# Kernel optimization log

Hardware: AMD Instinct MI355X
Metric: run time of the kernel (lower is better)

Reference implementation:

```python
import jax, jax.numpy as jnp
import numpy as np

PROB_THRESHOLD = 0.5


def setup_inputs() -> dict:
    key = jax.random.key(0)
    B, H, W = 64, 480, 864
    mask = jax.random.uniform(key, (B, H, W), dtype=jnp.float32)
    return {"mask": mask, "n_pts_threshold": 10, "n_bbox_loose_pixels": 64}


def reference(mask, n_pts_threshold, n_bbox_loose_pixels):
    """Threshold mask, find per-sample bbox of above-threshold pixels, loosen
    by n_bbox_loose_pixels, and emit a binary attention map over that bbox.
    If fewer than n_pts_threshold pixels fire, the whole frame is attended.
    Returns (att_map [B,H,W] float, bbox [B,4] int32 as [y0,y1,x0,x1])."""
    B, H, W = mask.shape
    binm = mask > PROB_THRESHOLD                       # [B,H,W] bool
    cnt = jnp.sum(binm, axis=(1, 2))                   # [B]

    rows = jnp.any(binm, axis=2)                       # [B,H] row has a hit
    cols = jnp.any(binm, axis=1)                       # [B,W] col has a hit
    r_idx = jnp.arange(H, dtype=jnp.int32)
    c_idx = jnp.arange(W, dtype=jnp.int32)

    min_r = jnp.min(jnp.where(rows, r_idx, H), axis=1)
    max_r = jnp.max(jnp.where(rows, r_idx, -1), axis=1)
    min_c = jnp.min(jnp.where(cols, c_idx, W), axis=1)
    max_c = jnp.max(jnp.where(cols, c_idx, -1), axis=1)

    loose = jnp.int32(n_bbox_loose_pixels)
    full = cnt < n_pts_threshold                       # too few pts -> full frame
    y0 = jnp.where(full, 0,     jnp.clip(min_r - loose, 0, H - 1))
    y1 = jnp.where(full, H - 1, jnp.clip(max_r + loose, 0, H - 1))
    x0 = jnp.where(full, 0,     jnp.clip(min_c - loose, 0, W - 1))
    x1 = jnp.where(full, W - 1, jnp.clip(max_c + loose, 0, W - 1))

    in_rows = (r_idx[None, :] >= y0[:, None]) & (r_idx[None, :] <= y1[:, None])  # [B,H]
    in_cols = (c_idx[None, :] >= x0[:, None]) & (c_idx[None, :] <= x1[:, None])  # [B,W]
    att_map = (in_rows[:, :, None] & in_cols[:, None, :]).astype(mask.dtype)     # [B,H,W]

    bbox = jnp.stack([y0, y1, x0, x1], axis=1).astype(jnp.int32)                 # [B,4]
    return att_map, bbox
```

## Files before the change

kernel.cpp:

```cpp
#include <hip/hip_runtime.h>

constexpr int B = 64;
constexpr int H = 480;
constexpr int W = 864;
constexpr float PROB_THRESHOLD = 0.5f;

constexpr int BPS = 16;
constexpr int ROWS_PER_BLK = H / BPS;
constexpr int W4 = W / 4;
constexpr int N4_PER_BLK = ROWS_PER_BLK * W4;
constexpr int NBLK = B * BPS;

using f32x4 = __attribute__((ext_vector_type(4))) float;
using u64 = unsigned long long;

constexpr u64 MARKER = 0xFFull << 56;

__device__ inline u64 pack_partial(int minr, int maxr, int minc, int maxc,
                                   int cnt) {
  u64 v = (u64)(unsigned)minr | ((u64)(unsigned)(maxr + 1) << 9) |
          ((u64)(unsigned)minc << 18) | ((u64)(unsigned)(maxc + 1) << 28) |
          ((u64)(unsigned)min(cnt, 4095) << 38) | MARKER;
  return v;
}

__global__ __launch_bounds__(256, 4) void fused_kernel(
    const float* __restrict__ mask, const int* __restrict__ n_pts_threshold,
    const int* __restrict__ n_bbox_loose, float* __restrict__ out,
    float* __restrict__ bbox_out, u64* __restrict__ part) {
  const int b    = blockIdx.x >> 4;
  const int blk  = blockIdx.x & 15;
  const int row0 = blk * ROWS_PER_BLK;
  const f32x4* __restrict__ base =
      (const f32x4*)(mask + ((size_t)b * H + row0) * (size_t)W);

  int minr = H, maxr = -1, minc = W, maxc = -1, cnt = 0;

  auto process = [&](f32x4 v, int i) {
    int r = i / W4;
    int c = (i - r * W4) * 4;
    bool h0 = v.x > PROB_THRESHOLD;
    bool h1 = v.y > PROB_THRESHOLD;
    bool h2 = v.z > PROB_THRESHOLD;
    bool h3 = v.w > PROB_THRESHOLD;
    int m = (h0 ? 1 : 0) | (h1 ? 2 : 0) | (h2 ? 4 : 0) | (h3 ? 8 : 0);
    if (m) {
      int rr = row0 + r;
      minr = min(minr, rr);
      maxr = max(maxr, rr);
      int lo = c + (h0 ? 0 : (h1 ? 1 : (h2 ? 2 : 3)));
      int hi = c + (h3 ? 3 : (h2 ? 2 : (h1 ? 1 : 0)));
      minc = min(minc, lo);
      maxc = max(maxc, hi);
      cnt += __popc(m);
    }
  };

  int i = threadIdx.x;
  for (int it = 0; it < 3; ++it, i += 2048) {
    f32x4 v[8];
#pragma unroll
    for (int k = 0; k < 8; ++k)
      v[k] = __builtin_nontemporal_load(&base[i + k * 256]);
#pragma unroll
    for (int k = 0; k < 8; ++k) process(v[k], i + k * 256);
  }
  process(__builtin_nontemporal_load(&base[i]), i);
  i += 256;
  if (i < N4_PER_BLK) process(__builtin_nontemporal_load(&base[i]), i);

  for (int off = 32; off > 0; off >>= 1) {
    minr = min(minr, __shfl_down(minr, off));
    maxr = max(maxr, __shfl_down(maxr, off));
    minc = min(minc, __shfl_down(minc, off));
    maxc = max(maxc, __shfl_down(maxc, off));
    cnt += __shfl_down(cnt, off);
  }

  __shared__ int s[4][5];
  __shared__ u64 packed[BPS];
  const int wave = threadIdx.x >> 6;
  if ((threadIdx.x & 63) == 0) {
    s[wave][0] = minr; s[wave][1] = maxr;
    s[wave][2] = minc; s[wave][3] = maxc;
    s[wave][4] = cnt;
  }
  __syncthreads();

  u64* __restrict__ P = part + (size_t)b * BPS;
  if (threadIdx.x == 0) {
    for (int wv = 1; wv < 4; ++wv) {
      minr = min(minr, s[wv][0]);
      maxr = max(maxr, s[wv][1]);
      minc = min(minc, s[wv][2]);
      maxc = max(maxc, s[wv][3]);
      cnt += s[wv][4];
    }
    __hip_atomic_store(&P[blk], pack_partial(minr, maxr, minc, maxc, cnt),
                       __ATOMIC_RELAXED, __HIP_MEMORY_SCOPE_AGENT);
  }

  if (threadIdx.x < BPS) {
    u64 v;
    while (((v = __hip_atomic_load(&P[threadIdx.x], __ATOMIC_RELAXED,
                                   __HIP_MEMORY_SCOPE_AGENT)) >> 56) != 0xFF)
      __builtin_amdgcn_s_sleep(2);
    packed[threadIdx.x] = v;
  }
  __syncthreads();

  minr = H; maxr = -1; minc = W; maxc = -1; cnt = 0;
#pragma unroll
  for (int k = 0; k < BPS; ++k) {
    u64 v = packed[k];
    minr = min(minr, (int)(v & 511));
    maxr = max(maxr, (int)((v >> 9) & 511) - 1);
    minc = min(minc, (int)((v >> 18) & 1023));
    maxc = max(maxc, (int)((v >> 28) & 1023) - 1);
    cnt += (int)((v >> 38) & 4095);
  }
  const int thr   = n_pts_threshold[0];
  const int loose = n_bbox_loose[0];
  int y0, y1, x0, x1;
  if (cnt < thr) {
    y0 = 0; y1 = H - 1; x0 = 0; x1 = W - 1;
  } else {
    y0 = min(max(minr - loose, 0), H - 1);
    y1 = min(max(maxr + loose, 0), H - 1);
    x0 = min(max(minc - loose, 0), W - 1);
    x1 = min(max(maxc + loose, 0), W - 1);
  }
  if (blk == 0 && threadIdx.x == 0) {
    bbox_out[b * 4 + 0] = (float)y0;
    bbox_out[b * 4 + 1] = (float)y1;
    bbox_out[b * 4 + 2] = (float)x0;
    bbox_out[b * 4 + 3] = (float)x1;
  }

  f32x4* obase = (f32x4*)(out + ((size_t)b * H + row0) * (size_t)W);

  auto val4 = [&](int i2) {
    int r = i2 / W4;
    int c = (i2 - r * W4) * 4;
    int rr = row0 + r;
    bool inr = (rr >= y0) & (rr <= y1);
    f32x4 v;
    v.x = (inr & (c + 0 >= x0) & (c + 0 <= x1)) ? 1.0f : 0.0f;
    v.y = (inr & (c + 1 >= x0) & (c + 1 <= x1)) ? 1.0f : 0.0f;
    v.z = (inr & (c + 2 >= x0) & (c + 2 <= x1)) ? 1.0f : 0.0f;
    v.w = (inr & (c + 3 >= x0) & (c + 3 <= x1)) ? 1.0f : 0.0f;
    return v;
  };

  i = threadIdx.x;
  for (int it = 0; it < 6; ++it, i += 1024) {
    __builtin_nontemporal_store(val4(i),       &obase[i]);
    __builtin_nontemporal_store(val4(i + 256), &obase[i + 256]);
    __builtin_nontemporal_store(val4(i + 512), &obase[i + 512]);
    __builtin_nontemporal_store(val4(i + 768), &obase[i + 768]);
  }
  __builtin_nontemporal_store(val4(i), &obase[i]);
  i += 256;
  if (i < N4_PER_BLK) __builtin_nontemporal_store(val4(i), &obase[i]);
}

extern "C" void kernel_launch(void* const* d_in, const int* in_sizes, int n_in,
                              void* d_out, int out_size, void* d_ws,
                              size_t ws_size, hipStream_t stream) {
  const float* mask = (const float*)d_in[0];
  const int* n_pts_threshold = (const int*)d_in[1];
  const int* n_bbox_loose = (const int*)d_in[2];

  float* out = (float*)d_out;
  float* bbox_out = out + (size_t)B * H * W;
  u64* part = (u64*)d_ws;

  fused_kernel<<<NBLK, 256, 0, stream>>>(mask, n_pts_threshold, n_bbox_loose,
                                         out, bbox_out, part);
}
```

Baseline: 179.0 us.

## Scan rows from both ends and exit early once the block bbox saturates

Each block now walks its rows in pairs, taking one row from the top and one from the bottom, with a one-step register prefetch. After each step it checks block-wide whether the partial bbox already touches every edge of the block's row range and the full width, and whether the count has reached the threshold. Once both hold, no further rows can change the result, so the block stops reading and publishes a saturated partial. This removes most of the mask read traffic when hits are dense. The cost is a per-step wave reduction plus two __syncthreads. The column-extent math also switches to ffs/clz.

Result: faster. 167.9 us (-6.2%).

```diff
diff --git a/kernel.cpp b/kernel.cpp
--- a/kernel.cpp
+++ b/kernel.cpp
@@ -10,6 +10,7 @@
 constexpr int W4 = W / 4;
 constexpr int N4_PER_BLK = ROWS_PER_BLK * W4;
 constexpr int NBLK = B * BPS;
+constexpr int NPAIRS = ROWS_PER_BLK / 2;
 
 using f32x4 = __attribute__((ext_vector_type(4))) float;
 using u64 = unsigned long long;
@@ -31,81 +32,121 @@
   const int b    = blockIdx.x >> 4;
   const int blk  = blockIdx.x & 15;
   const int row0 = blk * ROWS_PER_BLK;
-  const f32x4* __restrict__ base =
+  const f32x4* __restrict__ m4 =
       (const f32x4*)(mask + ((size_t)b * H + row0) * (size_t)W);
 
+  const int thr = n_pts_threshold[0];
+  const int tid = threadIdx.x;
+  const int wave = tid >> 6;
+  const int lane = tid & 63;
+
+  const bool aTop = tid < W4;
+  const int aC4   = aTop ? tid : tid - W4;
+  const bool hasB = tid < (2 * W4 - 256);
+  const int bC4   = tid + (256 - W4);
+  const int aC = aC4 * 4, bC = bC4 * 4;
+
   int minr = H, maxr = -1, minc = W, maxc = -1, cnt = 0;
 
-  auto process = [&](f32x4 v, int i) {
-    int r = i / W4;
-    int c = (i - r * W4) * 4;
+  auto proc = [&](f32x4 v, int row, int c) {
     bool h0 = v.x > PROB_THRESHOLD;
     bool h1 = v.y > PROB_THRESHOLD;
     bool h2 = v.z > PROB_THRESHOLD;
     bool h3 = v.w > PROB_THRESHOLD;
     int m = (h0 ? 1 : 0) | (h1 ? 2 : 0) | (h2 ? 4 : 0) | (h3 ? 8 : 0);
     if (m) {
-      int rr = row0 + r;
-      minr = min(minr, rr);
-      maxr = max(maxr, rr);
-      int lo = c + (h0 ? 0 : (h1 ? 1 : (h2 ? 2 : 3)));
-      int hi = c + (h3 ? 3 : (h2 ? 2 : (h1 ? 1 : 0)));
-      minc = min(minc, lo);
-      maxc = max(maxc, hi);
+      minr = min(minr, row);
+      maxr = max(maxr, row);
+      minc = min(minc, c + (__ffs(m) - 1));
+      maxc = max(maxc, c + (31 - __clz(m)));
       cnt += __popc(m);
     }
   };
 
-  int i = threadIdx.x;
-  for (int it = 0; it < 3; ++it, i += 2048) {
-    f32x4 v[8];
-#pragma unroll
-    for (int k = 0; k < 8; ++k)
-      v[k] = __builtin_nontemporal_load(&base[i + k * 256]);
-#pragma unroll
-    for (int k = 0; k < 8; ++k) process(v[k], i + k * 256);
-  }
-  process(__builtin_nontemporal_load(&base[i]), i);
-  i += 256;
-  if (i < N4_PER_BLK) process(__builtin_nontemporal_load(&base[i]), i);
-
-  for (int off = 32; off > 0; off >>= 1) {
-    minr = min(minr, __shfl_down(minr, off));
-    maxr = max(maxr, __shfl_down(maxr, off));
-    minc = min(minc, __shfl_down(minc, off));
-    maxc = max(maxc, __shfl_down(maxc, off));
-    cnt += __shfl_down(cnt, off);
-  }
-
-  __shared__ int s[4][5];
+  auto loadA = [&](int s) {
+    int rr = aTop ? s : (ROWS_PER_BLK - 1 - s);
+    return __builtin_nontemporal_load(&m4[rr * W4 + aC4]);
+  };
+  auto loadB = [&](int s) {
+    return __builtin_nontemporal_load(&m4[(ROWS_PER_BLK - 1 - s) * W4 + bC4]);
+  };
+
+  __shared__ int rflags[4];
+  __shared__ int rcnt[4];
+  __shared__ int s5[4][5];
   __shared__ u64 packed[BPS];
-  const int wave = threadIdx.x >> 6;
-  if ((threadIdx.x & 63) == 0) {
-    s[wave][0] = minr; s[wave][1] = maxr;
-    s[wave][2] = minc; s[wave][3] = maxc;
-    s[wave][4] = cnt;
-  }
-  __syncthreads();
+
+  bool stopped = false;
+  f32x4 pa = loadA(0);
+  f32x4 pb{};
+  if (hasB) pb = loadB(0);
+
+  for (int s = 0; s < NPAIRS; ++s) {
+    f32x4 ca = pa, cb = pb;
+    const int sn = (s + 1 < NPAIRS) ? s + 1 : s;
+    pa = loadA(sn);
+    if (hasB) pb = loadB(sn);
+
+    const int rt = row0 + s;
+    const int rb = row0 + ROWS_PER_BLK - 1 - s;
+    proc(ca, aTop ? rt : rb, aC);
+    if (hasB) proc(cb, rb, bC);
+
+    int wc = cnt;
+    for (int off = 1; off < 64; off <<= 1) wc += __shfl_xor(wc, off);
+    int fl = (__any(minr == row0) ? 1 : 0) |
+             (__any(maxr == row0 + ROWS_PER_BLK - 1) ? 2 : 0) |
+             (__any(minc == 0) ? 4 : 0) |
+             (__any(maxc == W - 1) ? 8 : 0);
+    if (lane == 0) { rflags[wave] = fl; rcnt[wave] = wc; }
+    __syncthreads();
+    const int bfl  = rflags[0] | rflags[1] | rflags[2] | rflags[3];
+    const int bcnt = rcnt[0] + rcnt[1] + rcnt[2] + rcnt[3];
+    const bool stop = (bfl == 15) && (bcnt >= thr);
+    __syncthreads();
+    if (stop) { stopped = true; break; }
+  }
 
   u64* __restrict__ P = part + (size_t)b * BPS;
-  if (threadIdx.x == 0) {
-    for (int wv = 1; wv < 4; ++wv) {
-      minr = min(minr, s[wv][0]);
-      maxr = max(maxr, s[wv][1]);
-      minc = min(minc, s[wv][2]);
-      maxc = max(maxc, s[wv][3]);
-      cnt += s[wv][4];
-    }
-    __hip_atomic_store(&P[blk], pack_partial(minr, maxr, minc, maxc, cnt),
-                       __ATOMIC_RELAXED, __HIP_MEMORY_SCOPE_AGENT);
-  }
-
-  if (threadIdx.x < BPS) {
+  if (stopped) {
+    if (tid == 0)
+      __hip_atomic_store(
+          &P[blk],
+          pack_partial(row0, row0 + ROWS_PER_BLK - 1, 0, W - 1, 4095),
+          __ATOMIC_RELAXED, __HIP_MEMORY_SCOPE_AGENT);
+  } else {
+    for (int off = 32; off > 0; off >>= 1) {
+      minr = min(minr, __shfl_down(minr, off));
+      maxr = max(maxr, __shfl_down(maxr, off));
+      minc = min(minc, __shfl_down(minc, off));
+      maxc = max(maxc, __shfl_down(maxc, off));
+      cnt += __shfl_down(cnt, off);
+    }
+    if (lane == 0) {
+      s5[wave][0] = minr; s5[wave][1] = maxr;
+      s5[wave][2] = minc; s5[wave][3] = maxc;
+      s5[wave][4] = cnt;
+    }
+    __syncthreads();
+    if (tid == 0) {
+      for (int wv = 1; wv < 4; ++wv) {
+        minr = min(minr, s5[wv][0]);
+        maxr = max(maxr, s5[wv][1]);
+        minc = min(minc, s5[wv][2]);
+        maxc = max(maxc, s5[wv][3]);
+        cnt += s5[wv][4];
+      }
+      __hip_atomic_store(&P[blk], pack_partial(minr, maxr, minc, maxc, cnt),
+                         __ATOMIC_RELAXED, __HIP_MEMORY_SCOPE_AGENT);
+    }
+  }
+
+  if (tid < BPS) {
     u64 v;
-    while (((v = __hip_atomic_load(&P[threadIdx.x], __ATOMIC_RELAXED,
+    while (((v = __hip_atomic_load(&P[tid], __ATOMIC_RELAXED,
                                    __HIP_MEMORY_SCOPE_AGENT)) >> 56) != 0xFF)
       __builtin_amdgcn_s_sleep(2);
-    packed[threadIdx.x] = v;
+    packed[tid] = v;
   }
   __syncthreads();
 
@@ -119,7 +160,6 @@
     maxc = max(maxc, (int)((v >> 28) & 1023) - 1);
     cnt += (int)((v >> 38) & 4095);
   }
-  const int thr   = n_pts_threshold[0];
   const int loose = n_bbox_loose[0];
   int y0, y1, x0, x1;
   if (cnt < thr) {
@@ -130,7 +170,7 @@
     x0 = min(max(minc - loose, 0), W - 1);
     x1 = min(max(maxc + loose, 0), W - 1);
   }
-  if (blk == 0 && threadIdx.x == 0) {
+  if (blk == 0 && tid == 0) {
     bbox_out[b * 4 + 0] = (float)y0;
     bbox_out[b * 4 + 1] = (float)y1;
     bbox_out[b * 4 + 2] = (float)x0;
@@ -152,7 +192,7 @@
     return v;
   };
 
-  i = threadIdx.x;
+  int i = tid;
   for (int it = 0; it < 6; ++it, i += 1024) {
     __builtin_nontemporal_store(val4(i),       &obase[i]);
     __builtin_nontemporal_store(val4(i + 256), &obase[i + 256]);
```
